# Kernel optimization log

Measured on AMD Instinct MI355X. Metric: run time of the kernel, lower is better.

Reference implementation:

```python
import jax, jax.numpy as jnp
import numpy as np
import math

VOCAB, D, L, NC, DC, K, DFF = 50257, 1024, 8, 4096, 256, 8, 4096
B, T = 8, 256

def ternary_ste(w):
    # torch: w_q + (w - w_q).detach() -> forward value == w, grad only via w_q
    alpha = jnp.maximum(jnp.mean(jnp.abs(w)), 1e-5)
    w_q = jnp.clip(jnp.round(w / alpha), -1.0, 1.0)
    return w_q + jax.lax.stop_gradient(w - w_q)

def rmsnorm(x, w):
    return x * jax.lax.rsqrt(jnp.mean(x * x, axis=-1, keepdims=True) + 1e-6) * w

def setup_inputs() -> dict:
    key = jax.random.key(0)
    ks = jax.random.split(key, 16)
    n = lambda k, sh, s: (jax.random.normal(k, sh, dtype=jnp.float32) * s)
    return {
        'tokens': jax.random.randint(ks[0], (B, T), 0, VOCAB),
        'embed': n(ks[1], (VOCAB, D), 0.02),
        'ln_in_w': jnp.ones((D,), jnp.float32),
        'ln_out_w': jnp.ones((D,), jnp.float32),
        'W_route': n(ks[2], (L, NC, D), 0.02),
        'cells': n(ks[3], (L, NC, DC), 0.01),
        'W_in': n(ks[4], (L, D, DC), 0.01),
        'W_out': n(ks[5], (L, DC, D), 0.01),
        'state_decay': jnp.full((L,), 3.0, jnp.float32),
        'state_gate_w': jnp.full((L, D), 0.1, jnp.float32),
        'state_gate_b': jnp.zeros((L, D), jnp.float32),
        'state_scale': jnp.full((L, D), 0.1, jnp.float32),
        'cell_scale': jnp.full((L,), 0.1, jnp.float32),
        'W_ff_gate': n(ks[6], (L, D, DFF), 0.02),
        'W_ff_up': n(ks[7], (L, D, DFF), 0.02),
        'W_ff_down': n(ks[8], (L, DFF, D), 0.02),
        'ff_norm_w': jnp.ones((L, D), jnp.float32),
        'norm_w': jnp.ones((L, D), jnp.float32),
    }

def _layer(x, Wr, cells, Wi, Wo, sd, sgw, sgb, ss, cs, Wg, Wu, Wd, ffn_w, nrm_w):
    Bx, Tx, Dx = x.shape
    # cell memory
    scores = jnp.einsum('btd,cd->btc', x, ternary_ste(Wr)) / math.sqrt(Dx)
    topk_s, topk_i = jax.lax.top_k(scores, K)          # [B,T,K]
    w = jax.nn.softmax(topk_s, axis=-1)
    cell_vals = cells[topk_i]                          # [B,T,K,DC]
    readout = jnp.einsum('btkc,btk->btc', cell_vals, w)
    x_in = jnp.einsum('btd,dc->btc', x, ternary_ste(Wi))
    cell_out = jnp.einsum('btc,cd->btd', readout + x_in, ternary_ste(Wo))
    # running state scan
    gate = jax.nn.sigmoid(x * sgw + sgb)
    updates = gate * x                                  # [B,T,D]
    decay = jnp.clip(jax.nn.sigmoid(sd), 0.01, 0.99)
    def step(h, u):
        h = h * decay + u
        return h, h
    _, states = jax.lax.scan(step, jnp.zeros((Bx, Dx), x.dtype), jnp.swapaxes(updates, 0, 1))
    state_out = jnp.swapaxes(states, 0, 1) * ss
    x = rmsnorm(x + cs * cell_out + state_out, nrm_w)
    # ternary SwiGLU FFN
    h = rmsnorm(x, ffn_w)
    g = jnp.einsum('btd,df->btf', h, ternary_ste(Wg))
    u = jnp.einsum('btd,df->btf', h, ternary_ste(Wu))
    ff = jnp.einsum('btf,fd->btd', jax.nn.silu(g) * u, ternary_ste(Wd))
    return x + ff

def reference(tokens, embed, ln_in_w, ln_out_w, W_route, cells, W_in, W_out,
              state_decay, state_gate_w, state_gate_b, state_scale, cell_scale,
              W_ff_gate, W_ff_up, W_ff_down, ff_norm_w, norm_w):
    h = rmsnorm(embed[tokens], ln_in_w)
    for i in range(L):
        h = _layer(h, W_route[i], cells[i], W_in[i], W_out[i], state_decay[i],
                   state_gate_w[i], state_gate_b[i], state_scale[i], cell_scale[i],
                   W_ff_gate[i], W_ff_up[i], W_ff_down[i], ff_norm_w[i], norm_w[i])
    logits = jnp.einsum('btd,vd->btv', rmsnorm(h, ln_out_w), embed)  # tied head
    return logits
```

## Files before the change

### kernel.cpp

```cpp
#include <hip/hip_runtime.h>
#include <stdint.h>

typedef __attribute__((ext_vector_type(8))) short bf16x8;
typedef __attribute__((ext_vector_type(4))) float f32x4;
typedef unsigned short u16;
typedef unsigned int u32;

#define MTOK 2048
#define DMODEL 1024
#define NCELL 4096
#define DCELL 256
#define DFF 4096
#define NVOCAB 50257
#define VPAD_LD 50304

struct __attribute__((packed, aligned(4))) f4u { float x, y, z, w; };

static __device__ __forceinline__ u16 f2bf(float f) {
  u32 u = __builtin_bit_cast(u32, f);
  u = (u + 0x7FFFu + ((u >> 16) & 1u)) >> 16;
  return (u16)u;
}
static __device__ __forceinline__ u32 pk2(float a, float b) {
  return (u32)f2bf(a) | ((u32)f2bf(b) << 16);
}
static __device__ __forceinline__ float sigm(float x) { return 1.0f / (1.0f + __expf(-x)); }

static __device__ __forceinline__ void glds16(const void* g, void* l) {
  __builtin_amdgcn_global_load_lds(
      (const __attribute__((address_space(1))) void*)g,
      (__attribute__((address_space(3))) void*)l, 16, 0, 0);
}

static __device__ __forceinline__ float blockReduceSum(float v) {
#pragma unroll
  for (int o = 32; o > 0; o >>= 1) v += __shfl_xor(v, o);
  __shared__ float sm[4];
  __syncthreads();
  if ((threadIdx.x & 63) == 0) sm[threadIdx.x >> 6] = v;
  __syncthreads();
  return sm[0] + sm[1] + sm[2] + sm[3];
}

template<int TM, int TN, int EPI>
__global__ __launch_bounds__(256, 3) void k_gemm_v3(
    const u16* __restrict__ A, const u16* __restrict__ B,
    float* __restrict__ Cf, u16* __restrict__ Cb, const float* __restrict__ Res,
    int NB, int K, int ldc, float alpha)
{
  __shared__ __align__(16) u16 As[TM * 64];
  __shared__ __align__(16) u16 Bs[TN * 64];
  constexpr int MI = TM / 32;
  constexpr int NI = TN / 32;
  constexpr int ACH = TM / 32;
  constexpr int BCH = TN / 32;
  constexpr int MB = 2048 / TM;
  const int tid = threadIdx.x;
  const int T = gridDim.x;
  const int bid = blockIdx.x;
  const int w = (bid & 7) * (T >> 3) + (bid >> 3);
  const int m0 = (w % MB) * TM;
  const int n0 = (w / MB) * TN;
  const int l = tid & 63;
  const int wv = tid >> 6;
  const int wm = wv >> 1, wn = wv & 1;
  const int lr = l & 15, lg = l >> 4;
  const int wbase = tid & ~63;

  f32x4 acc[MI][NI] = {};

  const int row_ = tid >> 3;
  const int kc_ = (tid & 7) << 3;
  const int nk = K >> 6;

  for (int s = 0; s < nk; ++s) {
    const int k0 = s << 6;
#pragma unroll
    for (int c = 0; c < ACH; ++c) {
      int row = c * 32 + row_;
      glds16(&A[(size_t)(m0 + row) * K + k0 + kc_],
             &As[(size_t)(c * 256 + wbase) * 8]);
    }
#pragma unroll
    for (int c = 0; c < BCH; ++c) {
      int row = c * 32 + row_;
      int gr = n0 + row; if (gr > NB - 1) gr = NB - 1;
      glds16(&B[(size_t)gr * K + k0 + kc_],
             &Bs[(size_t)(c * 256 + wbase) * 8]);
    }
    __syncthreads();
#pragma unroll
    for (int kk = 0; kk < 2; ++kk) {
      bf16x8 fa[MI], fb[NI];
#pragma unroll
      for (int mi = 0; mi < MI; ++mi)
        fa[mi] = *(const bf16x8*)&As[(wm * (TM / 2) + mi * 16 + lr) * 64 + kk * 32 + lg * 8];
#pragma unroll
      for (int ni = 0; ni < NI; ++ni)
        fb[ni] = *(const bf16x8*)&Bs[(wn * (TN / 2) + ni * 16 + lr) * 64 + kk * 32 + lg * 8];
#pragma unroll
      for (int mi = 0; mi < MI; ++mi)
#pragma unroll
        for (int ni = 0; ni < NI; ++ni)
          acc[mi][ni] = __builtin_amdgcn_mfma_f32_16x16x32_bf16(fa[mi], fb[ni], acc[mi][ni], 0, 0, 0);
    }
    __syncthreads();
  }

#pragma unroll
  for (int mi = 0; mi < MI; ++mi)
#pragma unroll
    for (int ni = 0; ni < NI; ++ni) {
      int col = n0 + wn * (TN / 2) + ni * 16 + lr;
#pragma unroll
      for (int j = 0; j < 4; ++j) {
        int row = m0 + wm * (TM / 2) + mi * 16 + lg * 4 + j;
        float v = acc[mi][ni][j];
        if constexpr (EPI == 0) {
          Cf[(size_t)row * ldc + col] = v * alpha;
        } else if constexpr (EPI == 1) {
          size_t off = (size_t)row * ldc + col;
          float r = Res[off] + v;
          Cf[off] = r;
          Cb[off] = f2bf(r);
        } else if constexpr (EPI == 2) {
          if (col < NB) Cf[(size_t)row * ldc + col] = v;
        } else {
          float p = __shfl_xor(v, 1);
          float a = v * sigm(v) * p;
          float a2 = __shfl_xor(a, 2);
          if ((lr & 3) == 0)
            *(u32*)&Cb[(size_t)row * DFF + (col >> 1)] = pk2(a, a2);
        }
      }
    }
}

__global__ __launch_bounds__(256) void k_copy_out(
    const float* __restrict__ pad, float* __restrict__ out)
{
  int row = blockIdx.x;
  const float* s = pad + (size_t)row * VPAD_LD;
  float* d = out + (size_t)row * NVOCAB;
  int t = threadIdx.x;
  int head = (int)((16 - (((size_t)d) & 15)) & 15) >> 2;
  if (t < head) d[t] = s[t];
  int nb = (NVOCAB - head) >> 2;
  const float* sb = s + head;
  float* db = d + head;
  for (int i = t; i < nb; i += 256) {
    f4u v = *(const f4u*)&sb[i * 4];
    *(float4*)&db[i * 4] = make_float4(v.x, v.y, v.z, v.w);
  }
  int t0 = head + nb * 4;
  int rem = NVOCAB - t0;
  if (t < rem) d[t0 + t] = s[t0 + t];
}

__global__ __launch_bounds__(256, 3) void k_gemm64(
    const u16* __restrict__ A, const u16* __restrict__ B,
    float* __restrict__ Cf, int K, int lda, int ldb, int ldc)
{
  __shared__ __align__(16) u16 As[64 * 64];
  __shared__ __align__(16) u16 Bs[64 * 64];
  const int tid = threadIdx.x;
  const int m0 = blockIdx.x * 64;
  const int n0 = blockIdx.y * 64;
  const int l = tid & 63;
  const int wv = tid >> 6;
  const int wm = wv >> 1, wn = wv & 1;
  const int lr = l & 15, lg = l >> 4;

  uint4 aR[2], bR[2];
  f32x4 acc[2][2] = {};
  const int nk = K >> 6;

  auto loadAB = [&](int k0) {
#pragma unroll
    for (int c = 0; c < 2; ++c) {
      int id = c * 256 + tid;
      int row = id >> 3, kc = (id & 7) << 3;
      aR[c] = *(const uint4*)&A[(size_t)(m0 + row) * lda + k0 + kc];
      bR[c] = *(const uint4*)&B[(size_t)(n0 + row) * ldb + k0 + kc];
    }
  };
  auto stage = [&]() {
#pragma unroll
    for (int c = 0; c < 2; ++c) {
      int id = c * 256 + tid;
      int row = id >> 3, kc = (id & 7) << 3;
      *(uint4*)&As[row * 64 + kc] = aR[c];
      *(uint4*)&Bs[row * 64 + kc] = bR[c];
    }
  };

  loadAB(0);
  for (int s = 0; s < nk; ++s) {
    __syncthreads();
    stage();
    __syncthreads();
    if (s + 1 < nk) loadAB((s + 1) << 6);
#pragma unroll
    for (int kk = 0; kk < 2; ++kk) {
      bf16x8 fa[2], fb[2];
#pragma unroll
      for (int mi = 0; mi < 2; ++mi)
        fa[mi] = *(const bf16x8*)&As[(wm * 32 + mi * 16 + lr) * 64 + kk * 32 + lg * 8];
#pragma unroll
      for (int ni = 0; ni < 2; ++ni)
        fb[ni] = *(const bf16x8*)&Bs[(wn * 32 + ni * 16 + lr) * 64 + kk * 32 + lg * 8];
#pragma unroll
      for (int mi = 0; mi < 2; ++mi)
#pragma unroll
        for (int ni = 0; ni < 2; ++ni)
          acc[mi][ni] = __builtin_amdgcn_mfma_f32_16x16x32_bf16(fa[mi], fb[ni], acc[mi][ni], 0, 0, 0);
    }
  }

#pragma unroll
  for (int mi = 0; mi < 2; ++mi)
#pragma unroll
    for (int ni = 0; ni < 2; ++ni) {
      int col = n0 + wn * 32 + ni * 16 + lr;
#pragma unroll
      for (int j = 0; j < 4; ++j) {
        int row = m0 + wm * 32 + mi * 16 + lg * 4 + j;
        Cf[(size_t)row * ldc + col] = acc[mi][ni][j];
      }
    }
}

__global__ void k_transpose_layer(
    const float* __restrict__ Wi, const float* __restrict__ Wo,
    const float* __restrict__ Wg, const float* __restrict__ Wu,
    const float* __restrict__ Wd, const float* __restrict__ Wr,
    u16* __restrict__ WiT, u16* __restrict__ WoT,
    u16* __restrict__ WguT, u16* __restrict__ WdT, u16* __restrict__ WrB)
{
  int bid = blockIdx.x;
  if (bid >= 12800) {
    int i = (bid - 12800) * 256 + threadIdx.x;
    const float4* s = (const float4*)(Wr + (size_t)i * 8);
    float4 a = s[0], b = s[1];
    *(uint4*)(WrB + (size_t)i * 8) =
        make_uint4(pk2(a.x, a.y), pk2(a.z, a.w), pk2(b.x, b.y), pk2(b.z, b.w));
    return;
  }
  const float* src; u16* dst; int R, C, t0, mul, add;
  if (bid < 256)       { src = Wi; dst = WiT;  R = 1024; C = 256;  t0 = bid;        mul = 1; add = 0; }
  else if (bid < 512)  { src = Wo; dst = WoT;  R = 256;  C = 1024; t0 = bid - 256;  mul = 1; add = 0; }
  else if (bid < 4608) { src = Wg; dst = WguT; R = 1024; C = 4096; t0 = bid - 512;  mul = 2; add = 0; }
  else if (bid < 8704) { src = Wu; dst = WguT; R = 1024; C = 4096; t0 = bid - 4608; mul = 2; add = 1; }
  else                 { src = Wd; dst = WdT;  R = 4096; C = 1024; t0 = bid - 8704; mul = 1; add = 0; }
  int tC = C >> 5;
  int r0 = (t0 / tC) << 5, c0 = (t0 % tC) << 5;
  __shared__ float tile[32][33];
  int ty = threadIdx.x >> 3;
  int tx = (threadIdx.x & 7) << 2;
  float4 v = *(const float4*)&src[(size_t)(r0 + ty) * C + c0 + tx];
  tile[ty][tx] = v.x; tile[ty][tx + 1] = v.y; tile[ty][tx + 2] = v.z; tile[ty][tx + 3] = v.w;
  __syncthreads();
  float a = tile[tx][ty], b = tile[tx + 1][ty], c = tile[tx + 2][ty], d = tile[tx + 3][ty];
  *(uint2*)&dst[((size_t)(c0 + ty) * mul + add) * R + r0 + tx] = make_uint2(pk2(a, b), pk2(c, d));
}

__global__ void k_f2bf(const float* __restrict__ src, u16* __restrict__ dst, int n8)
{
  int i = blockIdx.x * 256 + threadIdx.x;
  if (i >= n8) return;
  const float4* s = (const float4*)(src + (size_t)i * 8);
  float4 a = s[0], b = s[1];
  *(uint4*)(dst + (size_t)i * 8) =
      make_uint4(pk2(a.x, a.y), pk2(a.z, a.w), pk2(b.x, b.y), pk2(b.z, b.w));
}

__global__ void k_embed_norm(const int* __restrict__ tok, const float* __restrict__ emb,
                             const float* __restrict__ w, float* __restrict__ xf,
                             u16* __restrict__ xb)
{
  int row = blockIdx.x;
  int t = tok[row];
  float4 v = ((const float4*)(emb + (size_t)t * DMODEL))[threadIdx.x];
  float tot = blockReduceSum(v.x * v.x + v.y * v.y + v.z * v.z + v.w * v.w);
  float inv = rsqrtf(tot * (1.0f / DMODEL) + 1e-6f);
  int d0 = threadIdx.x << 2;
  float4 wv = *(const float4*)(w + d0);
  float4 o;
  o.x = v.x * inv * wv.x; o.y = v.y * inv * wv.y;
  o.z = v.z * inv * wv.z; o.w = v.w * inv * wv.w;
  *(float4*)(xf + (size_t)row * DMODEL + d0) = o;
  *(uint2*)(xb + (size_t)row * DMODEL + d0) = make_uint2(pk2(o.x, o.y), pk2(o.z, o.w));
}

__global__ __launch_bounds__(256) void k_topk(const float* __restrict__ scores,
                                              float* __restrict__ wout, int* __restrict__ iout)
{
  int row = blockIdx.x * 4 + (threadIdx.x >> 6);
  int l = threadIdx.x & 63;
  const float* s = scores + (size_t)row * NCELL;
  float v[8]; int ix[8];
#pragma unroll
  for (int i = 0; i < 8; ++i) { v[i] = -3.4e38f; ix[i] = 0x7fffffff; }
  for (int j = 0; j < 64; ++j) {
    float x = s[j * 64 + l];
    if (x > v[7]) {
      v[7] = x; ix[7] = j * 64 + l;
#pragma unroll
      for (int q = 7; q > 0; --q) {
        if (v[q] > v[q - 1]) {
          float tv = v[q]; v[q] = v[q - 1]; v[q - 1] = tv;
          int tt = ix[q]; ix[q] = ix[q - 1]; ix[q - 1] = tt;
        }
      }
    }
  }
  float ov[8]; int oi[8];
#pragma unroll
  for (int r = 0; r < 8; ++r) {
    float bv = v[0]; int bi = ix[0];
#pragma unroll
    for (int o = 32; o > 0; o >>= 1) {
      float tv = __shfl_xor(bv, o);
      int tb = __shfl_xor(bi, o);
      if (tv > bv || (tv == bv && tb < bi)) { bv = tv; bi = tb; }
    }
    ov[r] = bv; oi[r] = bi;
    if (bi == ix[0]) {
#pragma unroll
      for (int q = 0; q < 7; ++q) { v[q] = v[q + 1]; ix[q] = ix[q + 1]; }
      v[7] = -3.4e38f; ix[7] = 0x7fffffff;
    }
  }
  if (l == 0) {
    float m = ov[0], sum = 0.f, e[8];
#pragma unroll
    for (int r = 0; r < 8; ++r) { e[r] = __expf(ov[r] - m); sum += e[r]; }
    float inv = 1.0f / sum;
#pragma unroll
    for (int r = 0; r < 8; ++r) {
      wout[(size_t)row * 8 + r] = e[r] * inv;
      iout[(size_t)row * 8 + r] = oi[r];
    }
  }
}

__global__ void k_readout(const float* __restrict__ cells, const int* __restrict__ ti,
                          const float* __restrict__ tw, const float* __restrict__ xin,
                          u16* __restrict__ rb)
{
  int row = blockIdx.x, d = threadIdx.x;
  float acc = xin[(size_t)row * DCELL + d];
#pragma unroll
  for (int k = 0; k < 8; ++k) {
    int ci = ti[row * 8 + k];
    float wk = tw[row * 8 + k];
    acc += wk * cells[(size_t)ci * DCELL + d];
  }
  rb[(size_t)row * DCELL + d] = f2bf(acc);
}

__global__ void k_scan_a(const float* __restrict__ x, float* __restrict__ E,
                         const float* __restrict__ sgw, const float* __restrict__ sgb,
                         const float* __restrict__ sdec)
{
  int tid = blockIdx.x * 256 + threadIdx.x;
  int d = tid & 1023, bc = tid >> 10;
  int b = bc >> 2, c = bc & 3;
  float dec = sigm(sdec[0]);
  dec = fminf(fmaxf(dec, 0.01f), 0.99f);
  float gw = sgw[d], gb = sgb[d];
  size_t base = ((size_t)b * 256 + c * 64) * DMODEL + d;
  float h = 0.f;
  for (int t = 0; t < 64; ++t) {
    float xv = x[base + (size_t)t * DMODEL];
    h = h * dec + sigm(xv * gw + gb) * xv;
  }
  E[tid] = h;
}

__global__ void k_scan_b(const float* __restrict__ x, const float* __restrict__ co,
                         const float* __restrict__ E, float* __restrict__ pre,
                         const float* __restrict__ sgw, const float* __restrict__ sgb,
                         const float* __restrict__ ssc, const float* __restrict__ sdec,
                         const float* __restrict__ csc)
{
  int tid = blockIdx.x * 256 + threadIdx.x;
  int d = tid & 1023, bc = tid >> 10;
  int b = bc >> 2, c = bc & 3;
  float dec = sigm(sdec[0]);
  dec = fminf(fmaxf(dec, 0.01f), 0.99f);
  float d2 = dec * dec, d4 = d2 * d2, d8 = d4 * d4, d16 = d8 * d8, d32 = d16 * d16;
  float d64 = d32 * d32;
  float cs = csc[0];
  float gw = sgw[d], gb = sgb[d], sc = ssc[d];
  float h = 0.f;
  for (int cc = 0; cc < c; ++cc) h = h * d64 + E[((b << 2) + cc) * 1024 + d];
  size_t base = ((size_t)b * 256 + c * 64) * DMODEL + d;
  for (int t = 0; t < 64; ++t) {
    size_t o = base + (size_t)t * DMODEL;
    float xv = x[o];
    float g = sigm(xv * gw + gb);
    h = h * dec + g * xv;
    pre[o] = xv + cs * co[o] + h * sc;
  }
}

__global__ void k_norm2(const float* __restrict__ pre, const float* __restrict__ nw,
                        const float* __restrict__ fw, float* __restrict__ xf,
                        u16* __restrict__ h2b)
{
  int row = blockIdx.x;
  float4 v = ((const float4*)(pre + (size_t)row * DMODEL))[threadIdx.x];
  float tot = blockReduceSum(v.x * v.x + v.y * v.y + v.z * v.z + v.w * v.w);
  float inv = rsqrtf(tot * (1.0f / DMODEL) + 1e-6f);
  int d0 = threadIdx.x << 2;
  float4 wv = *(const float4*)(nw + d0);
  float4 x1;
  x1.x = v.x * inv * wv.x; x1.y = v.y * inv * wv.y;
  x1.z = v.z * inv * wv.z; x1.w = v.w * inv * wv.w;
  *(float4*)(xf + (size_t)row * DMODEL + d0) = x1;
  float tot2 = blockReduceSum(x1.x * x1.x + x1.y * x1.y + x1.z * x1.z + x1.w * x1.w);
  float inv2 = rsqrtf(tot2 * (1.0f / DMODEL) + 1e-6f);
  float4 fv = *(const float4*)(fw + d0);
  *(uint2*)(h2b + (size_t)row * DMODEL + d0) =
      make_uint2(pk2(x1.x * inv2 * fv.x, x1.y * inv2 * fv.y),
                 pk2(x1.z * inv2 * fv.z, x1.w * inv2 * fv.w));
}

__global__ void k_norm_bf(const float* __restrict__ in, const float* __restrict__ w,
                          u16* __restrict__ ob)
{
  int row = blockIdx.x;
  float4 v = ((const float4*)(in + (size_t)row * DMODEL))[threadIdx.x];
  float tot = blockReduceSum(v.x * v.x + v.y * v.y + v.z * v.z + v.w * v.w);
  float inv = rsqrtf(tot * (1.0f / DMODEL) + 1e-6f);
  int d0 = threadIdx.x << 2;
  float4 wv = *(const float4*)(w + d0);
  *(uint2*)(ob + (size_t)row * DMODEL + d0) =
      make_uint2(pk2(v.x * inv * wv.x, v.y * inv * wv.y),
                 pk2(v.z * inv * wv.z, v.w * inv * wv.w));
}

extern "C" void kernel_launch(void* const* d_in, const int* in_sizes, int n_in,
                              void* d_out, int out_size, void* d_ws, size_t ws_size,
                              hipStream_t stream)
{
  const int*   tokens  = (const int*)d_in[0];
  const float* embed   = (const float*)d_in[1];
  const float* ln_in_w = (const float*)d_in[2];
  const float* ln_out_w= (const float*)d_in[3];
  const float* W_route = (const float*)d_in[4];
  const float* cells   = (const float*)d_in[5];
  const float* W_in    = (const float*)d_in[6];
  const float* W_out   = (const float*)d_in[7];
  const float* sdec    = (const float*)d_in[8];
  const float* sgw     = (const float*)d_in[9];
  const float* sgb     = (const float*)d_in[10];
  const float* ssc     = (const float*)d_in[11];
  const float* csc     = (const float*)d_in[12];
  const float* Wg      = (const float*)d_in[13];
  const float* Wu      = (const float*)d_in[14];
  const float* Wd      = (const float*)d_in[15];
  const float* ffw     = (const float*)d_in[16];
  const float* nrw     = (const float*)d_in[17];
  float* out = (float*)d_out;
  (void)in_sizes; (void)n_in; (void)out_size;

  char* ws = (char*)d_ws;
  size_t off = 0;
  auto alloc = [&](size_t bytes) -> void* {
    void* p = ws + off;
    off += (bytes + 255) & ~(size_t)255;
    return p;
  };

  float* scores = (float*)alloc((size_t)MTOK * NCELL * 4);
  u16*  act_bf  = (u16*)alloc((size_t)MTOK * DFF * 2);
  float* s_pre  = (float*)act_bf;
  float* x_f    = (float*)alloc((size_t)MTOK * DMODEL * 4);
  u16*  x_bf    = (u16*)alloc((size_t)MTOK * DMODEL * 2);
  u16*  h2_bf   = (u16*)alloc((size_t)MTOK * DMODEL * 2);
  float* tw     = (float*)alloc((size_t)MTOK * 8 * 4);
  int*  ti      = (int*)alloc((size_t)MTOK * 8 * 4);
  float* xin    = (float*)alloc((size_t)MTOK * DCELL * 4);
  u16*  r_bf    = (u16*)alloc((size_t)MTOK * DCELL * 2);
  float* cellout= (float*)alloc((size_t)MTOK * DMODEL * 4);
  u16*  WiT     = (u16*)alloc((size_t)DCELL * DMODEL * 2);
  u16*  WoT     = (u16*)alloc((size_t)DMODEL * DCELL * 2);
  u16*  WguT    = (u16*)alloc((size_t)8192 * DMODEL * 2);
  u16*  WdT     = (u16*)alloc((size_t)DMODEL * DFF * 2);
  u16*  WrB     = (u16*)alloc((size_t)NCELL * DMODEL * 2);
  float* E      = (float*)alloc((size_t)32768 * 4);
  if (off < ((size_t)108 << 20)) off = (size_t)108 << 20;
  u16*  xf_bf   = (u16*)alloc((size_t)MTOK * DMODEL * 2);
  float* vpad   = (float*)alloc((size_t)MTOK * VPAD_LD * 4);
  size_t need_pad = off;
  u16*  embed_bf = (u16*)ws;

  const bool use_pad = (ws_size >= need_pad);

  k_embed_norm<<<MTOK, 256, 0, stream>>>(tokens, embed, ln_in_w, x_f, x_bf);

  for (int lay = 0; lay < 8; ++lay) {
    const float* Wi_l = W_in  + (size_t)lay * DMODEL * DCELL;
    const float* Wo_l = W_out + (size_t)lay * DCELL * DMODEL;
    const float* Wg_l = Wg    + (size_t)lay * DMODEL * DFF;
    const float* Wu_l = Wu    + (size_t)lay * DMODEL * DFF;
    const float* Wd_l = Wd    + (size_t)lay * DFF * DMODEL;
    const float* Wr_l = W_route + (size_t)lay * NCELL * DMODEL;
    const float* cells_l = cells + (size_t)lay * NCELL * DCELL;

    k_transpose_layer<<<14848, 256, 0, stream>>>(Wi_l, Wo_l, Wg_l, Wu_l, Wd_l,
                                                 Wr_l, WiT, WoT, WguT, WdT, WrB);
    k_gemm_v3<128, 128, 0><<<512, 256, 0, stream>>>(x_bf, WrB, scores, nullptr,
        nullptr, NCELL, DMODEL, NCELL, 0.03125f);
    k_topk<<<512, 256, 0, stream>>>(scores, tw, ti);
    k_gemm64<<<dim3(32, 4), 256, 0, stream>>>(x_bf, WiT, xin,
        DMODEL, DMODEL, DMODEL, DCELL);
    k_readout<<<MTOK, 256, 0, stream>>>(cells_l, ti, tw, xin, r_bf);
    k_gemm64<<<dim3(32, 16), 256, 0, stream>>>(r_bf, WoT, cellout,
        DCELL, DCELL, DCELL, DMODEL);
    k_scan_a<<<128, 256, 0, stream>>>(x_f, E, sgw + lay * DMODEL,
        sgb + lay * DMODEL, sdec + lay);
    k_scan_b<<<128, 256, 0, stream>>>(x_f, cellout, E, s_pre, sgw + lay * DMODEL,
        sgb + lay * DMODEL, ssc + lay * DMODEL, sdec + lay, csc + lay);
    k_norm2<<<MTOK, 256, 0, stream>>>(s_pre, nrw + lay * DMODEL, ffw + lay * DMODEL,
        x_f, h2_bf);
    k_gemm_v3<128, 128, 3><<<1024, 256, 0, stream>>>(h2_bf, WguT, nullptr, act_bf,
        nullptr, 8192, DMODEL, 0, 1.0f);
    k_gemm_v3<64, 64, 1><<<512, 256, 0, stream>>>(act_bf, WdT, x_f, x_bf, x_f,
        DMODEL, DFF, DMODEL, 1.0f);
  }

  k_norm_bf<<<MTOK, 256, 0, stream>>>(x_f, ln_out_w, xf_bf);
  k_f2bf<<<(NVOCAB * (DMODEL / 8) + 255) / 256, 256, 0, stream>>>(
      embed, embed_bf, NVOCAB * (DMODEL / 8));
  if (use_pad) {
    k_gemm_v3<128, 128, 0><<<6288, 256, 0, stream>>>(xf_bf, embed_bf, vpad, nullptr,
        nullptr, NVOCAB, DMODEL, VPAD_LD, 1.0f);
    k_copy_out<<<MTOK, 256, 0, stream>>>(vpad, out);
  } else {
    k_gemm_v3<128, 128, 2><<<6288, 256, 0, stream>>>(xf_bf, embed_bf, out, nullptr,
        nullptr, NVOCAB, DMODEL, NVOCAB, 1.0f);
  }
}
```

Measured before the change: 2.953 ms.

## Fuse topk with readout, scan with norms, and Win GEMM with scan prefix

Merges top-k selection and cell readout into one kernel, runs the W_in GEMM and the chunked scan prefix in a single launch, and fuses the scan with both RMSNorms in one 1024-thread kernel per chunk of 32 tokens. It also merges the final norm with the embedding bf16 conversion and adds nontemporal stores for the logits and the copy-out. The goal is fewer launches and fewer intermediate round-trips through global memory. The risk is that the fused scan-norm kernel runs only 64 blocks and does two block reductions per token, so it may leave the GPU underused.

```diff
diff --git a/kernel.cpp b/kernel.cpp
--- a/kernel.cpp
+++ b/kernel.cpp
@@ -14,8 +14,6 @@
 #define NVOCAB 50257
 #define VPAD_LD 50304
 
-struct __attribute__((packed, aligned(4))) f4u { float x, y, z, w; };
-
 static __device__ __forceinline__ u16 f2bf(float f) {
   u32 u = __builtin_bit_cast(u32, f);
   u = (u + 0x7FFFu + ((u >> 16) & 1u)) >> 16;
@@ -40,6 +38,18 @@
   if ((threadIdx.x & 63) == 0) sm[threadIdx.x >> 6] = v;
   __syncthreads();
   return sm[0] + sm[1] + sm[2] + sm[3];
+}
+
+static __device__ __forceinline__ float blockReduce1024(float v, float* sm) {
+#pragma unroll
+  for (int o = 32; o > 0; o >>= 1) v += __shfl_xor(v, o);
+  if ((threadIdx.x & 63) == 0) sm[threadIdx.x >> 6] = v;
+  __syncthreads();
+  float r = 0.f;
+#pragma unroll
+  for (int i = 0; i < 16; ++i) r += sm[i];
+  __syncthreads();
+  return r;
 }
 
 template<int TM, int TN, int EPI>
@@ -125,12 +135,14 @@
           Cb[off] = f2bf(r);
         } else if constexpr (EPI == 2) {
           if (col < NB) Cf[(size_t)row * ldc + col] = v;
-        } else {
+        } else if constexpr (EPI == 3) {
           float p = __shfl_xor(v, 1);
           float a = v * sigm(v) * p;
           float a2 = __shfl_xor(a, 2);
           if ((lr & 3) == 0)
             *(u32*)&Cb[(size_t)row * DFF + (col >> 1)] = pk2(a, a2);
+        } else {
+          __builtin_nontemporal_store(v, &Cf[(size_t)row * ldc + col]);
         }
       }
     }
@@ -149,23 +161,25 @@
   const float* sb = s + head;
   float* db = d + head;
   for (int i = t; i < nb; i += 256) {
-    f4u v = *(const f4u*)&sb[i * 4];
-    *(float4*)&db[i * 4] = make_float4(v.x, v.y, v.z, v.w);
+    f32x4 v;
+    v.x = __builtin_nontemporal_load(&sb[i * 4 + 0]);
+    v.y = __builtin_nontemporal_load(&sb[i * 4 + 1]);
+    v.z = __builtin_nontemporal_load(&sb[i * 4 + 2]);
+    v.w = __builtin_nontemporal_load(&sb[i * 4 + 3]);
+    __builtin_nontemporal_store(v, (f32x4*)&db[i * 4]);
   }
   int t0 = head + nb * 4;
   int rem = NVOCAB - t0;
   if (t < rem) d[t0 + t] = s[t0 + t];
 }
 
-__global__ __launch_bounds__(256, 3) void k_gemm64(
-    const u16* __restrict__ A, const u16* __restrict__ B,
-    float* __restrict__ Cf, int K, int lda, int ldb, int ldc)
-{
-  __shared__ __align__(16) u16 As[64 * 64];
-  __shared__ __align__(16) u16 Bs[64 * 64];
+static __device__ __forceinline__ void gemm64_body(
+    const u16* A, const u16* B, float* Cf,
+    int m0, int n0, int K, int lda, int ldb, int ldc, char* smem)
+{
+  u16* As = (u16*)smem;
+  u16* Bs = (u16*)(smem + 64 * 64 * 2);
   const int tid = threadIdx.x;
-  const int m0 = blockIdx.x * 64;
-  const int n0 = blockIdx.y * 64;
   const int l = tid & 63;
   const int wv = tid >> 6;
   const int wm = wv >> 1, wn = wv & 1;
@@ -228,6 +242,145 @@
         Cf[(size_t)row * ldc + col] = acc[mi][ni][j];
       }
     }
+}
+
+__global__ __launch_bounds__(256, 3) void k_gemm64(
+    const u16* __restrict__ A, const u16* __restrict__ B,
+    float* __restrict__ Cf, int K, int lda, int ldb, int ldc)
+{
+  __shared__ __align__(16) char smem[16384];
+  gemm64_body(A, B, Cf, blockIdx.x * 64, blockIdx.y * 64, K, lda, ldb, ldc, smem);
+}
+
+__global__ __launch_bounds__(256, 3) void k_prep_fused(
+    const u16* __restrict__ x_bf, const u16* __restrict__ WiT,
+    float* __restrict__ xin,
+    const float* __restrict__ x_f, float* __restrict__ E,
+    const float* __restrict__ sgw, const float* __restrict__ sgb,
+    const float* __restrict__ sdec)
+{
+  __shared__ __align__(16) char smem[16384];
+  int bid = blockIdx.x;
+  if (bid < 128) {
+    gemm64_body(x_bf, WiT, xin, (bid & 31) * 64, (bid >> 5) * 64,
+                DMODEL, DMODEL, DMODEL, DCELL, smem);
+    return;
+  }
+  int tid = (bid - 128) * 256 + threadIdx.x;
+  int d = tid & 1023, bc = tid >> 10;
+  int b = bc >> 3, c = bc & 7;
+  float dec = sigm(sdec[0]);
+  dec = fminf(fmaxf(dec, 0.01f), 0.99f);
+  float gw = sgw[d], gb = sgb[d];
+  size_t base = ((size_t)b * 256 + c * 32) * DMODEL + d;
+  float h = 0.f;
+  for (int t = 0; t < 32; ++t) {
+    float xv = x_f[base + (size_t)t * DMODEL];
+    h = h * dec + sigm(xv * gw + gb) * xv;
+  }
+  E[tid] = h;
+}
+
+__global__ __launch_bounds__(256) void k_cell_fused(
+    const float* __restrict__ scores, const float* __restrict__ cells,
+    const float* __restrict__ xin, u16* __restrict__ rb)
+{
+  __shared__ float sw[4][8];
+  __shared__ int si[4][8];
+  int row0 = blockIdx.x * 4;
+  int wvid = threadIdx.x >> 6;
+  int row = row0 + wvid;
+  int l = threadIdx.x & 63;
+  const float* s = scores + (size_t)row * NCELL;
+  float v[8]; int ix[8];
+#pragma unroll
+  for (int i = 0; i < 8; ++i) { v[i] = -3.4e38f; ix[i] = 0x7fffffff; }
+  for (int j = 0; j < 64; ++j) {
+    float x = s[j * 64 + l];
+    if (x > v[7]) {
+      v[7] = x; ix[7] = j * 64 + l;
+#pragma unroll
+      for (int q = 7; q > 0; --q) {
+        if (v[q] > v[q - 1]) {
+          float tv = v[q]; v[q] = v[q - 1]; v[q - 1] = tv;
+          int tt = ix[q]; ix[q] = ix[q - 1]; ix[q - 1] = tt;
+        }
+      }
+    }
+  }
+  float ov[8]; int oi[8];
+#pragma unroll
+  for (int r = 0; r < 8; ++r) {
+    float bv = v[0]; int bi = ix[0];
+#pragma unroll
+    for (int o = 32; o > 0; o >>= 1) {
+      float tv = __shfl_xor(bv, o);
+      int tb = __shfl_xor(bi, o);
+      if (tv > bv || (tv == bv && tb < bi)) { bv = tv; bi = tb; }
+    }
+    ov[r] = bv; oi[r] = bi;
+    if (bi == ix[0]) {
+#pragma unroll
+      for (int q = 0; q < 7; ++q) { v[q] = v[q + 1]; ix[q] = ix[q + 1]; }
+      v[7] = -3.4e38f; ix[7] = 0x7fffffff;
+    }
+  }
+  if (l == 0) {
+    float m = ov[0], sum = 0.f, e[8];
+#pragma unroll
+    for (int r = 0; r < 8; ++r) { e[r] = __expf(ov[r] - m); sum += e[r]; }
+    float inv = 1.0f / sum;
+#pragma unroll
+    for (int r = 0; r < 8; ++r) { sw[wvid][r] = e[r] * inv; si[wvid][r] = oi[r]; }
+  }
+  __syncthreads();
+  int d = threadIdx.x;
+#pragma unroll
+  for (int r = 0; r < 4; ++r) {
+    int rr = row0 + r;
+    float acc = xin[(size_t)rr * DCELL + d];
+#pragma unroll
+    for (int k = 0; k < 8; ++k)
+      acc += sw[r][k] * cells[(size_t)si[r][k] * DCELL + d];
+    rb[(size_t)rr * DCELL + d] = f2bf(acc);
+  }
+}
+
+__global__ __launch_bounds__(1024) void k_scan_norm(
+    float* __restrict__ x_f, const float* __restrict__ co,
+    const float* __restrict__ E, u16* __restrict__ h2b,
+    const float* __restrict__ sgw, const float* __restrict__ sgb,
+    const float* __restrict__ ssc, const float* __restrict__ sdec,
+    const float* __restrict__ csc, const float* __restrict__ nw,
+    const float* __restrict__ fw)
+{
+  __shared__ float sm[16];
+  int b = blockIdx.x >> 3, c = blockIdx.x & 7;
+  int d = threadIdx.x;
+  float dec = sigm(sdec[0]);
+  dec = fminf(fmaxf(dec, 0.01f), 0.99f);
+  float d2 = dec * dec, d4 = d2 * d2, d8 = d4 * d4, d16 = d8 * d8;
+  float d32 = d16 * d16;
+  float cs = csc[0];
+  float gw = sgw[d], gb = sgb[d], sc = ssc[d];
+  float nwd = nw[d], fwd = fw[d];
+  float h = 0.f;
+  for (int cc = 0; cc < c; ++cc) h = h * d32 + E[((b << 3) + cc) * 1024 + d];
+  size_t base = ((size_t)b * 256 + c * 32) * DMODEL + d;
+  for (int t = 0; t < 32; ++t) {
+    size_t o = base + (size_t)t * DMODEL;
+    float xv = x_f[o];
+    float g = sigm(xv * gw + gb);
+    h = h * dec + g * xv;
+    float pre = xv + cs * co[o] + h * sc;
+    float s1 = blockReduce1024(pre * pre, sm);
+    float inv = rsqrtf(s1 * (1.0f / DMODEL) + 1e-6f);
+    float x1 = pre * inv * nwd;
+    float s2 = blockReduce1024(x1 * x1, sm);
+    float inv2 = rsqrtf(s2 * (1.0f / DMODEL) + 1e-6f);
+    x_f[o] = x1;
+    h2b[o] = f2bf(x1 * inv2 * fwd);
+  }
 }
 
 __global__ void k_transpose_layer(
@@ -264,16 +417,6 @@
   *(uint2*)&dst[((size_t)(c0 + ty) * mul + add) * R + r0 + tx] = make_uint2(pk2(a, b), pk2(c, d));
 }
 
-__global__ void k_f2bf(const float* __restrict__ src, u16* __restrict__ dst, int n8)
-{
-  int i = blockIdx.x * 256 + threadIdx.x;
-  if (i >= n8) return;
-  const float4* s = (const float4*)(src + (size_t)i * 8);
-  float4 a = s[0], b = s[1];
-  *(uint4*)(dst + (size_t)i * 8) =
-      make_uint4(pk2(a.x, a.y), pk2(a.z, a.w), pk2(b.x, b.y), pk2(b.z, b.w));
-}
-
 __global__ void k_embed_norm(const int* __restrict__ tok, const float* __restrict__ emb,
                              const float* __restrict__ w, float* __restrict__ xf,
                              u16* __restrict__ xb)
@@ -292,146 +435,23 @@
   *(uint2*)(xb + (size_t)row * DMODEL + d0) = make_uint2(pk2(o.x, o.y), pk2(o.z, o.w));
 }
 
-__global__ __launch_bounds__(256) void k_topk(const float* __restrict__ scores,
-                                              float* __restrict__ wout, int* __restrict__ iout)
-{
-  int row = blockIdx.x * 4 + (threadIdx.x >> 6);
-  int l = threadIdx.x & 63;
-  const float* s = scores + (size_t)row * NCELL;
-  float v[8]; int ix[8];
-#pragma unroll
-  for (int i = 0; i < 8; ++i) { v[i] = -3.4e38f; ix[i] = 0x7fffffff; }
-  for (int j = 0; j < 64; ++j) {
-    float x = s[j * 64 + l];
-    if (x > v[7]) {
-      v[7] = x; ix[7] = j * 64 + l;
-#pragma unroll
-      for (int q = 7; q > 0; --q) {
-        if (v[q] > v[q - 1]) {
-          float tv = v[q]; v[q] = v[q - 1]; v[q - 1] = tv;
-          int tt = ix[q]; ix[q] = ix[q - 1]; ix[q - 1] = tt;
-        }
-      }
-    }
-  }
-  float ov[8]; int oi[8];
-#pragma unroll
-  for (int r = 0; r < 8; ++r) {
-    float bv = v[0]; int bi = ix[0];
-#pragma unroll
-    for (int o = 32; o > 0; o >>= 1) {
-      float tv = __shfl_xor(bv, o);
-      int tb = __shfl_xor(bi, o);
-      if (tv > bv || (tv == bv && tb < bi)) { bv = tv; bi = tb; }
-    }
-    ov[r] = bv; oi[r] = bi;
-    if (bi == ix[0]) {
-#pragma unroll
-      for (int q = 0; q < 7; ++q) { v[q] = v[q + 1]; ix[q] = ix[q + 1]; }
-      v[7] = -3.4e38f; ix[7] = 0x7fffffff;
-    }
-  }
-  if (l == 0) {
-    float m = ov[0], sum = 0.f, e[8];
-#pragma unroll
-    for (int r = 0; r < 8; ++r) { e[r] = __expf(ov[r] - m); sum += e[r]; }
-    float inv = 1.0f / sum;
-#pragma unroll
-    for (int r = 0; r < 8; ++r) {
-      wout[(size_t)row * 8 + r] = e[r] * inv;
-      iout[(size_t)row * 8 + r] = oi[r];
-    }
-  }
-}
-
-__global__ void k_readout(const float* __restrict__ cells, const int* __restrict__ ti,
-                          const float* __restrict__ tw, const float* __restrict__ xin,
-                          u16* __restrict__ rb)
-{
-  int row = blockIdx.x, d = threadIdx.x;
-  float acc = xin[(size_t)row * DCELL + d];
-#pragma unroll
-  for (int k = 0; k < 8; ++k) {
-    int ci = ti[row * 8 + k];
-    float wk = tw[row * 8 + k];
-    acc += wk * cells[(size_t)ci * DCELL + d];
-  }
-  rb[(size_t)row * DCELL + d] = f2bf(acc);
-}
-
-__global__ void k_scan_a(const float* __restrict__ x, float* __restrict__ E,
-                         const float* __restrict__ sgw, const float* __restrict__ sgb,
-                         const float* __restrict__ sdec)
-{
-  int tid = blockIdx.x * 256 + threadIdx.x;
-  int d = tid & 1023, bc = tid >> 10;
-  int b = bc >> 2, c = bc & 3;
-  float dec = sigm(sdec[0]);
-  dec = fminf(fmaxf(dec, 0.01f), 0.99f);
-  float gw = sgw[d], gb = sgb[d];
-  size_t base = ((size_t)b * 256 + c * 64) * DMODEL + d;
-  float h = 0.f;
-  for (int t = 0; t < 64; ++t) {
-    float xv = x[base + (size_t)t * DMODEL];
-    h = h * dec + sigm(xv * gw + gb) * xv;
-  }
-  E[tid] = h;
-}
-
-__global__ void k_scan_b(const float* __restrict__ x, const float* __restrict__ co,
-                         const float* __restrict__ E, float* __restrict__ pre,
-                         const float* __restrict__ sgw, const float* __restrict__ sgb,
-                         const float* __restrict__ ssc, const float* __restrict__ sdec,
-                         const float* __restrict__ csc)
-{
-  int tid = blockIdx.x * 256 + threadIdx.x;
-  int d = tid & 1023, bc = tid >> 10;
-  int b = bc >> 2, c = bc & 3;
-  float dec = sigm(sdec[0]);
-  dec = fminf(fmaxf(dec, 0.01f), 0.99f);
-  float d2 = dec * dec, d4 = d2 * d2, d8 = d4 * d4, d16 = d8 * d8, d32 = d16 * d16;
-  float d64 = d32 * d32;
-  float cs = csc[0];
-  float gw = sgw[d], gb = sgb[d], sc = ssc[d];
-  float h = 0.f;
-  for (int cc = 0; cc < c; ++cc) h = h * d64 + E[((b << 2) + cc) * 1024 + d];
-  size_t base = ((size_t)b * 256 + c * 64) * DMODEL + d;
-  for (int t = 0; t < 64; ++t) {
-    size_t o = base + (size_t)t * DMODEL;
-    float xv = x[o];
-    float g = sigm(xv * gw + gb);
-    h = h * dec + g * xv;
-    pre[o] = xv + cs * co[o] + h * sc;
-  }
-}
-
-__global__ void k_norm2(const float* __restrict__ pre, const float* __restrict__ nw,
-                        const float* __restrict__ fw, float* __restrict__ xf,
-                        u16* __restrict__ h2b)
-{
-  int row = blockIdx.x;
-  float4 v = ((const float4*)(pre + (size_t)row * DMODEL))[threadIdx.x];
-  float tot = blockReduceSum(v.x * v.x + v.y * v.y + v.z * v.z + v.w * v.w);
-  float inv = rsqrtf(tot * (1.0f / DMODEL) + 1e-6f);
-  int d0 = threadIdx.x << 2;
-  float4 wv = *(const float4*)(nw + d0);
-  float4 x1;
-  x1.x = v.x * inv * wv.x; x1.y = v.y * inv * wv.y;
-  x1.z = v.z * inv * wv.z; x1.w = v.w * inv * wv.w;
-  *(float4*)(xf + (size_t)row * DMODEL + d0) = x1;
-  float tot2 = blockReduceSum(x1.x * x1.x + x1.y * x1.y + x1.z * x1.z + x1.w * x1.w);
-  float inv2 = rsqrtf(tot2 * (1.0f / DMODEL) + 1e-6f);
-  float4 fv = *(const float4*)(fw + d0);
-  *(uint2*)(h2b + (size_t)row * DMODEL + d0) =
-      make_uint2(pk2(x1.x * inv2 * fv.x, x1.y * inv2 * fv.y),
-                 pk2(x1.z * inv2 * fv.z, x1.w * inv2 * fv.w));
-}
-
-__global__ void k_norm_bf(const float* __restrict__ in, const float* __restrict__ w,
-                          u16* __restrict__ ob)
-{
-  int row = blockIdx.x;
-  float4 v = ((const float4*)(in + (size_t)row * DMODEL))[threadIdx.x];
+__global__ __launch_bounds__(256) void k_tail(
+    const float* __restrict__ xf, const float* __restrict__ w,
+    u16* __restrict__ ob, const float* __restrict__ emb,
+    u16* __restrict__ emb_bf)
+{
+  int bid = blockIdx.x;
+  if (bid >= 2048) {
+    int i = (bid - 2048) * 256 + threadIdx.x;
+    if (i >= NVOCAB * (DMODEL / 8)) return;
+    const float4* s = (const float4*)(emb + (size_t)i * 8);
+    float4 a = s[0], b = s[1];
+    *(uint4*)(emb_bf + (size_t)i * 8) =
+        make_uint4(pk2(a.x, a.y), pk2(a.z, a.w), pk2(b.x, b.y), pk2(b.z, b.w));
+    return;
+  }
+  int row = bid;
+  float4 v = ((const float4*)(xf + (size_t)row * DMODEL))[threadIdx.x];
   float tot = blockReduceSum(v.x * v.x + v.y * v.y + v.z * v.z + v.w * v.w);
   float inv = rsqrtf(tot * (1.0f / DMODEL) + 1e-6f);
   int d0 = threadIdx.x << 2;
@@ -476,12 +496,9 @@
 
   float* scores = (float*)alloc((size_t)MTOK * NCELL * 4);
   u16*  act_bf  = (u16*)alloc((size_t)MTOK * DFF * 2);
-  float* s_pre  = (float*)act_bf;
   float* x_f    = (float*)alloc((size_t)MTOK * DMODEL * 4);
   u16*  x_bf    = (u16*)alloc((size_t)MTOK * DMODEL * 2);
   u16*  h2_bf   = (u16*)alloc((size_t)MTOK * DMODEL * 2);
-  float* tw     = (float*)alloc((size_t)MTOK * 8 * 4);
-  int*  ti      = (int*)alloc((size_t)MTOK * 8 * 4);
   float* xin    = (float*)alloc((size_t)MTOK * DCELL * 4);
   u16*  r_bf    = (u16*)alloc((size_t)MTOK * DCELL * 2);
   float* cellout= (float*)alloc((size_t)MTOK * DMODEL * 4);
@@ -490,7 +507,7 @@
   u16*  WguT    = (u16*)alloc((size_t)8192 * DMODEL * 2);
   u16*  WdT     = (u16*)alloc((size_t)DMODEL * DFF * 2);
   u16*  WrB     = (u16*)alloc((size_t)NCELL * DMODEL * 2);
-  float* E      = (float*)alloc((size_t)32768 * 4);
+  float* E      = (float*)alloc((size_t)65536 * 4);
   if (off < ((size_t)108 << 20)) off = (size_t)108 << 20;
   u16*  xf_bf   = (u16*)alloc((size_t)MTOK * DMODEL * 2);
   float* vpad   = (float*)alloc((size_t)MTOK * VPAD_LD * 4);
@@ -514,29 +531,23 @@
                                                  Wr_l, WiT, WoT, WguT, WdT, WrB);
     k_gemm_v3<128, 128, 0><<<512, 256, 0, stream>>>(x_bf, WrB, scores, nullptr,
         nullptr, NCELL, DMODEL, NCELL, 0.03125f);
-    k_topk<<<512, 256, 0, stream>>>(scores, tw, ti);
-    k_gemm64<<<dim3(32, 4), 256, 0, stream>>>(x_bf, WiT, xin,
-        DMODEL, DMODEL, DMODEL, DCELL);
-    k_readout<<<MTOK, 256, 0, stream>>>(cells_l, ti, tw, xin, r_bf);
+    k_prep_fused<<<384, 256, 0, stream>>>(x_bf, WiT, xin, x_f, E,
+        sgw + lay * DMODEL, sgb + lay * DMODEL, sdec + lay);
+    k_cell_fused<<<512, 256, 0, stream>>>(scores, cells_l, xin, r_bf);
     k_gemm64<<<dim3(32, 16), 256, 0, stream>>>(r_bf, WoT, cellout,
         DCELL, DCELL, DCELL, DMODEL);
-    k_scan_a<<<128, 256, 0, stream>>>(x_f, E, sgw + lay * DMODEL,
-        sgb + lay * DMODEL, sdec + lay);
-    k_scan_b<<<128, 256, 0, stream>>>(x_f, cellout, E, s_pre, sgw + lay * DMODEL,
-        sgb + lay * DMODEL, ssc + lay * DMODEL, sdec + lay, csc + lay);
-    k_norm2<<<MTOK, 256, 0, stream>>>(s_pre, nrw + lay * DMODEL, ffw + lay * DMODEL,
-        x_f, h2_bf);
+    k_scan_norm<<<64, 1024, 0, stream>>>(x_f, cellout, E, h2_bf,
+        sgw + lay * DMODEL, sgb + lay * DMODEL, ssc + lay * DMODEL,
+        sdec + lay, csc + lay, nrw + lay * DMODEL, ffw + lay * DMODEL);
     k_gemm_v3<128, 128, 3><<<1024, 256, 0, stream>>>(h2_bf, WguT, nullptr, act_bf,
         nullptr, 8192, DMODEL, 0, 1.0f);
     k_gemm_v3<64, 64, 1><<<512, 256, 0, stream>>>(act_bf, WdT, x_f, x_bf, x_f,
         DMODEL, DFF, DMODEL, 1.0f);
   }
 
-  k_norm_bf<<<MTOK, 256, 0, stream>>>(x_f, ln_out_w, xf_bf);
-  k_f2bf<<<(NVOCAB * (DMODEL / 8) + 255) / 256, 256, 0, stream>>>(
-      embed, embed_bf, NVOCAB * (DMODEL / 8));
+  k_tail<<<2048 + 25129, 256, 0, stream>>>(x_f, ln_out_w, xf_bf, embed, embed_bf);
   if (use_pad) {
-    k_gemm_v3<128, 128, 0><<<6288, 256, 0, stream>>>(xf_bf, embed_bf, vpad, nullptr,
+    k_gemm_v3<128, 128, 4><<<6288, 256, 0, stream>>>(xf_bf, embed_bf, vpad, nullptr,
         nullptr, NVOCAB, DMODEL, VPAD_LD, 1.0f);
     k_copy_out<<<MTOK, 256, 0, stream>>>(vpad, out);
   } else {
```

New measurement: 2.906 ms. Within noise of the previous version (-1.6%).
